# Performance work log

Hardware: AMD Instinct MI355X
Metric: run time of the kernel (lower is better)

## Reference

```python
import jax, jax.numpy as jnp
import numpy as np

EPS = 1e-5


def spectral_conv3d(x, w):
    # x: [B, C, X, Y, Z] real; w: [4, Cin, Cout, m1, m2, m3, 2] (4 frequency corners, real/imag)
    m1, m2, m3 = w.shape[3], w.shape[4], w.shape[5]
    wc = w[..., 0] + 1j * w[..., 1]
    X, Y, Z = x.shape[-3], x.shape[-2], x.shape[-1]
    xf = jnp.fft.rfftn(x, axes=(-3, -2, -1), norm="ortho")  # [B,C,X,Y,Z//2+1] complex
    mul = lambda a, b: jnp.einsum('bixyz,ioxyz->boxyz', a, b)
    out = jnp.zeros(xf.shape, dtype=xf.dtype)
    out = out.at[:, :, :m1, :m2, :m3].set(mul(xf[:, :, :m1, :m2, :m3], wc[0]))
    out = out.at[:, :, -m1:, :m2, :m3].set(mul(xf[:, :, -m1:, :m2, :m3], wc[1]))
    out = out.at[:, :, :m1, -m2:, :m3].set(mul(xf[:, :, :m1, -m2:, :m3], wc[2]))
    out = out.at[:, :, -m1:, -m2:, :m3].set(mul(xf[:, :, -m1:, -m2:, :m3], wc[3]))
    return jnp.fft.irfftn(out, s=(X, Y, Z), axes=(-3, -2, -1), norm="ortho")


def batchnorm3d(x, g, b):
    # training-mode BatchNorm3d: stats over (B, X, Y, Z) per channel, biased variance
    mean = jnp.mean(x, axis=(0, 2, 3, 4), keepdims=True)
    var = jnp.var(x, axis=(0, 2, 3, 4), keepdims=True)
    xhat = (x - mean) * jax.lax.rsqrt(var + EPS)
    return xhat * g[None, :, None, None, None] + b[None, :, None, None, None]


def setup_inputs() -> dict:
    key = jax.random.key(0)
    ks = jax.random.split(key, 12)
    B, X, Y, Z = 4, 64, 64, 64
    W, M = 32, 8
    scale = 1.0 / (W * W)
    return {
        "x": jax.random.normal(ks[0], (B, X, Y, Z, 3), dtype=jnp.float32),
        "fc0_w": jax.random.normal(ks[1], (W, 3), dtype=jnp.float32) * 0.3,
        "fc0_b": jax.random.normal(ks[2], (W,), dtype=jnp.float32) * 0.1,
        "sw": scale * jax.random.uniform(ks[3], (4, 4, W, W, M, M, M, 2), dtype=jnp.float32),
        "cw": jax.random.normal(ks[4], (4, W, W), dtype=jnp.float32) * (1.0 / np.sqrt(W)),
        "cb": jax.random.normal(ks[5], (4, W), dtype=jnp.float32) * 0.05,
        "gamma": jnp.ones((4, W), dtype=jnp.float32),
        "beta": jnp.zeros((4, W), dtype=jnp.float32),
        "fc1_w": jax.random.normal(ks[6], (128, W), dtype=jnp.float32) * (1.0 / np.sqrt(W)),
        "fc1_b": jax.random.normal(ks[7], (128,), dtype=jnp.float32) * 0.05,
        "fc2_w": jax.random.normal(ks[8], (1, 128), dtype=jnp.float32) * (1.0 / np.sqrt(128.0)),
        "fc2_b": jax.random.normal(ks[9], (1,), dtype=jnp.float32) * 0.05,
    }


def reference(x, fc0_w, fc0_b, sw, cw, cb, gamma, beta, fc1_w, fc1_b, fc2_w, fc2_b):
    # lift: [B,X,Y,Z,3] -> [B,X,Y,Z,W] -> [B,W,X,Y,Z]
    h = jnp.einsum('bxyzi,wi->bxyzw', x, fc0_w) + fc0_b
    h = jnp.transpose(h, (0, 4, 1, 2, 3))
    for i in range(4):
        x1 = spectral_conv3d(h, sw[i])
        x2 = jnp.einsum('bcxyz,oc->boxyz', h, cw[i]) + cb[i][None, :, None, None, None]
        h = batchnorm3d(x1 + x2, gamma[i], beta[i])
        if i < 3:
            h = jax.nn.relu(h)
    h = jnp.transpose(h, (0, 2, 3, 4, 1))  # [B,X,Y,Z,W]
    h = jax.nn.relu(jnp.einsum('bxyzw,fw->bxyzf', h, fc1_w) + fc1_b)
    out = jnp.einsum('bxyzf,of->bxyzo', h, fc2_w) + fc2_b
    return out
```

## Files before the change

### kernel.cpp

```cpp
#include <hip/hip_runtime.h>

#define TW_STEP 0.09817477042468103f

typedef __bf16 bf16x8 __attribute__((ext_vector_type(8)));
typedef __bf16 bf16x4 __attribute__((ext_vector_type(4)));
typedef __bf16 bf16x2 __attribute__((ext_vector_type(2)));
typedef float  f32x4  __attribute__((ext_vector_type(4)));

static constexpr size_t SZ_P   = (size_t)4*32*64*64*64*2;
static constexpr size_t SZ_A   = (size_t)4*32*8*64*64*8;
static constexpr size_t SZ_B2  = (size_t)4*32*8*16*64*8;
static constexpr size_t SZ_XF  = (size_t)4*32*8*16*16*8;
static constexpr size_t OFF_P  = 0;
static constexpr size_t OFF_A  = OFF_P + SZ_P;
static constexpr size_t OFF_B2 = OFF_A + SZ_A;
static constexpr size_t OFF_XF = OFF_B2 + SZ_B2;
static constexpr size_t OFF_YF = OFF_XF + SZ_XF;
static constexpr size_t OFF_TW  = OFF_YF + SZ_XF;
static constexpr size_t OFF_BNP = OFF_TW + 512;
static constexpr size_t OFF_W1B = OFF_BNP + 1024;
static constexpr size_t OFF_B1P = OFF_W1B + 8192;
static constexpr size_t OFF_WFZ = OFF_B1P + 512;
static constexpr size_t OFF_WZ  = OFF_WFZ + 4096;
static constexpr size_t OFF_WY  = OFF_WZ + 8192;


__global__ void k_twinit(float2* tw, __bf16* wfz, __bf16* wz, __bf16* wy) {
    int t = threadIdx.x;
    if (t < 64) { float s, c; sincosf(TW_STEP * t, &s, &c); tw[t] = make_float2(c, s); }
    for (int e = t; e < 1024; e += 256) {
        int half = e >> 9, rem = e & 511, kg = rem >> 7, tt = (rem >> 3) & 15, j = e & 7;
        int z = half * 32 + kg * 8 + j, k = tt >> 1;
        float ang = TW_STEP * (float)((k * z) & 63);
        float val = (tt & 1) ? -sinf(ang) : cosf(ang);
        __bf16 hi = (__bf16)val;
        wfz[e] = hi;
        wfz[1024 + e] = (__bf16)(val - (float)hi);
    }
    for (int e = t; e < 2048; e += 256) {
        int z = e >> 5, tt = e & 31, k = tt >> 1;
        float ang = TW_STEP * (float)((k * z) & 63);
        float val;
        if (tt == 0) val = 1.f;
        else if (tt == 1) val = 0.f;
        else val = (tt & 1) ? (-2.f * sinf(ang)) : (2.f * cosf(ang));
        __bf16 hi = (__bf16)val;
        wz[e] = hi;
        wz[2048 + e] = (__bf16)(val - (float)hi);
    }
    for (int e = t; e < 4096; e += 256) {
        int j = e & 7, l = (e >> 3) & 63, hl = (e >> 9) & 1, nt = (e >> 10) & 1, kc = (e >> 11) & 1;
        int f = l & 15;
        int F = f < 8 ? f : f + 48;
        int y = kc * 32 + ((l >> 4) & 3) * 8 + j;
        float ang = TW_STEP * (float)((F * y) & 63);
        float val = nt ? sinf(ang) : cosf(ang);
        __bf16 hi = (__bf16)val;
        wy[e] = hl ? (__bf16)(val - (float)hi) : hi;
    }
}

__global__ __launch_bounds__(256) void k_lift(const float* __restrict__ x,
                                              const float* __restrict__ w,
                                              const float* __restrict__ bias,
                                              __bf16* __restrict__ P) {
    int v = blockIdx.x * 256 + threadIdx.x;
    int z = v & 63, y = (v >> 6) & 63, xx = (v >> 12) & 63, b = v >> 18;
    float i0 = x[(size_t)v * 3 + 0], i1 = x[(size_t)v * 3 + 1], i2 = x[(size_t)v * 3 + 2];
#pragma unroll
    for (int c = 0; c < 32; c++) {
        float val = bias[c] + w[c * 3 + 0] * i0 + w[c * 3 + 1] * i1 + w[c * 3 + 2] * i2;
        P[(size_t)(((b * 32 + c) * 64 + xx) * 64 + y) * 64 + z] = (__bf16)val;
    }
}

__global__ __launch_bounds__(256) void k_zfwd2(const __bf16* __restrict__ P,
                                               const __bf16* __restrict__ wfz,
                                               const __bf16* __restrict__ wy,
                                               const float* __restrict__ bnp, int relu,
                                               unsigned* __restrict__ T2u) {
    int blk = blockIdx.x;
    int x = blk & 63, c = (blk >> 6) & 31, b = blk >> 11;
    __shared__ __bf16 hs2buf[64][72];
    __shared__ float ttmp[16][66];
    __shared__ __bf16 af[16][72];
    float (*ddsh)[2][16][18] = (float(*)[2][16][18])hs2buf;
    int tid = threadIdx.x, l = tid & 63, w = tid >> 6;
    {
        int y = tid >> 2, q = tid & 3;
        float scb = 1.f, shb = 0.f;
        if (bnp) { scb = bnp[c]; shb = bnp[32 + c]; }
        const __bf16* src = P + ((size_t)((b * 32 + c) * 64 + x) * 64 + y) * 64 + q * 16;
        bf16x8 v0 = ((const bf16x8*)src)[0], v1 = ((const bf16x8*)src)[1];
        bf16x8 o0, o1;
#pragma unroll
        for (int j = 0; j < 8; j++) {
            float a = (float)v0[j], bb = (float)v1[j];
            if (bnp) {
                a = fmaf(a, scb, shb); bb = fmaf(bb, scb, shb);
                if (relu) { a = fmaxf(a, 0.f); bb = fmaxf(bb, 0.f); }
            }
            o0[j] = (__bf16)a; o1[j] = (__bf16)bb;
        }
        *(bf16x8*)&hs2buf[y][q * 16] = o0;
        *(bf16x8*)&hs2buf[y][q * 16 + 8] = o1;
    }
    __syncthreads();
    int col = l & 15, kg = l >> 4;
    {
        f32x4 acc = (f32x4){0.f, 0.f, 0.f, 0.f};
#pragma unroll
        for (int half = 0; half < 2; half++) {
            bf16x8 a = *(const bf16x8*)&hs2buf[w * 16 + col][half * 32 + kg * 8];
            const __bf16* wp = wfz + ((half * 4 + kg) * 16 + col) * 8;
            bf16x8 bh = *(const bf16x8*)wp;
            bf16x8 blo = *(const bf16x8*)(wp + 1024);
            acc = __builtin_amdgcn_mfma_f32_16x16x32_bf16(a, bh, acc, 0, 0, 0);
            acc = __builtin_amdgcn_mfma_f32_16x16x32_bf16(a, blo, acc, 0, 0, 0);
        }
#pragma unroll
        for (int r = 0; r < 4; r++) ttmp[col][w * 16 + kg * 4 + r] = acc[r];
    }
    __syncthreads();
    {
        int row = tid >> 4, yq = tid & 15;
        float v0 = ttmp[row][yq * 4 + 0];
        float v1 = ttmp[row][yq * 4 + 1];
        float v2 = ttmp[row][yq * 4 + 2];
        float v3 = ttmp[row][yq * 4 + 3];
        bf16x4 o;
        o[0] = (__bf16)v0; o[1] = (__bf16)v1; o[2] = (__bf16)v2; o[3] = (__bf16)v3;
        *(bf16x4*)&af[row][yq * 4] = o;
    }
    __syncthreads();
    {
        int nt = w & 1, kc = w >> 1;
        bf16x8 a = *(const bf16x8*)&af[col][kc * 32 + kg * 8];
        const __bf16* wp = wy + (kc * 2 + nt) * 1024 + l * 8;
        bf16x8 bh = *(const bf16x8*)wp;
        bf16x8 blo = *(const bf16x8*)(wp + 512);
        f32x4 d = (f32x4){0.f, 0.f, 0.f, 0.f};
        d = __builtin_amdgcn_mfma_f32_16x16x32_bf16(a, bh, d, 0, 0, 0);
        d = __builtin_amdgcn_mfma_f32_16x16x32_bf16(a, blo, d, 0, 0, 0);
#pragma unroll
        for (int r = 0; r < 4; r++) ddsh[kc][nt][kg * 4 + r][col] = d[r];
    }
    __syncthreads();
    if (tid < 128) {
        int kz = tid >> 4, f = tid & 15;
        int tre = 2 * kz, tim = 2 * kz + 1;
        float Re = (ddsh[0][0][tre][f] + ddsh[1][0][tre][f])
                 + (ddsh[0][1][tim][f] + ddsh[1][1][tim][f]);
        float Im = (ddsh[0][0][tim][f] + ddsh[1][0][tim][f])
                 - (ddsh[0][1][tre][f] + ddsh[1][1][tre][f]);
        union { __bf16 h[2]; unsigned u; } pk;
        pk.h[0] = (__bf16)Re; pk.h[1] = (__bf16)Im;
        T2u[(size_t)((b * 32 + c) * 8 + kz) * 1024 + f * 64 + x] = pk.u;
    }
}

__global__ __launch_bounds__(256) void k_dftm(const __bf16* __restrict__ in,
                                              float2* __restrict__ outf,
                                              const __bf16* __restrict__ wy) {
    int rb = blockIdx.x * 16;
    __shared__ __bf16 af[32 * 72];
    __shared__ float dd[2][2][16][18];
    int tid = threadIdx.x, l = tid & 63, w = tid >> 6;
    {
        int r = tid >> 4, yq = tid & 15;
        bf16x8 v = *(const bf16x8*)(in + ((size_t)(rb + r) * 64 + yq * 4) * 2);
        bf16x4 re, im;
#pragma unroll
        for (int j = 0; j < 4; j++) { re[j] = v[2 * j]; im[j] = v[2 * j + 1]; }
        *(bf16x4*)&af[(2 * r) * 72 + yq * 4] = re;
        *(bf16x4*)&af[(2 * r + 1) * 72 + yq * 4] = im;
    }
    __syncthreads();
    int mt = w >> 1, nt = w & 1, col = l & 15, kg = l >> 4;
    f32x4 acc = (f32x4){0.f, 0.f, 0.f, 0.f};
#pragma unroll
    for (int kc = 0; kc < 2; kc++) {
        bf16x8 a = *(const bf16x8*)&af[(mt * 16 + col) * 72 + kc * 32 + kg * 8];
        const __bf16* wp = wy + (kc * 2 + nt) * 1024 + l * 8;
        bf16x8 bh = *(const bf16x8*)wp;
        bf16x8 blo = *(const bf16x8*)(wp + 512);
        acc = __builtin_amdgcn_mfma_f32_16x16x32_bf16(a, bh, acc, 0, 0, 0);
        acc = __builtin_amdgcn_mfma_f32_16x16x32_bf16(a, blo, acc, 0, 0, 0);
    }
#pragma unroll
    for (int r = 0; r < 4; r++) dd[mt][nt][kg * 4 + r][col] = acc[r];
    __syncthreads();
    {
        int cr = tid >> 4, f = tid & 15;
        int mt2 = cr >> 3, tre = (2 * cr) & 15, tim = (2 * cr + 1) & 15;
        float Re = dd[mt2][0][tre][f] + dd[mt2][1][tim][f];
        float Im = dd[mt2][0][tim][f] - dd[mt2][1][tre][f];
        int rg = rb + cr;
        outf[rg * 16 + f] = make_float2(Re, Im);
    }
}

__global__ __launch_bounds__(128) void k_specmul(const float2* __restrict__ Xf,
                                                 const float* __restrict__ swl,
                                                 float2* __restrict__ Yf) {
    int m = blockIdx.x;
    int kxi = m & 15, kyi = (m >> 4) & 15, kz = m >> 8;
    int corner = (kxi >= 8 ? 1 : 0) + (kyi >= 8 ? 2 : 0);
    int mx = kxi & 7, my = kyi & 7;
    __shared__ float2 wsd[1024];
    __shared__ float2 xfs[128];
    int tid = threadIdx.x;
    const float* wb = swl + (size_t)corner * 1048576 + mx * 128 + my * 16 + kz * 2;
    for (int idx = tid; idx < 1024; idx += 128) {
        int i = idx >> 5, o = idx & 31;
        const float* p = wb + (size_t)i * 32768 + o * 1024;
        wsd[idx] = make_float2(p[0], p[1]);
    }
    {
        int b = tid >> 5, i = tid & 31;
        xfs[tid] = Xf[(((b * 32 + i) * 8 + kz) * 16 + kyi) * 16 + kxi];
    }
    __syncthreads();
    int b = tid >> 5, o = tid & 31;
    float ar = 0.f, ai = 0.f;
#pragma unroll
    for (int i = 0; i < 32; i++) {
        float2 xv = xfs[b * 32 + i];
        float2 wv = wsd[i * 32 + o];
        ar += xv.x * wv.x - xv.y * wv.y;
        ai += xv.x * wv.y + xv.y * wv.x;
    }
    const float s = 1.0f / 262144.0f;
    Yf[(((b * 32 + o) * 8 + kz) * 16 + kyi) * 16 + kxi] = make_float2(ar * s, ai * s);
}

__global__ __launch_bounds__(256) void k_xinv(const float2* __restrict__ Yf,
                                              unsigned* __restrict__ U1p) {
    int blk = blockIdx.x;
    int kz = blk & 7, o = (blk >> 3) & 31, b = blk >> 8;
    __shared__ float2 yfs[16][17];
    __shared__ float2 tw[64];
    int tid = threadIdx.x;
    if (tid < 64) { float s, c; sincosf(TW_STEP * tid, &s, &c); tw[tid] = make_float2(c, s); }
    {
        int kyi = tid >> 4, kxi = tid & 15;
        yfs[kyi][kxi] = Yf[(size_t)((b * 32 + o) * 8 + kz) * 256 + tid];
    }
    __syncthreads();
    size_t base = (size_t)((b * 8 + kz) * 64) * 512 + o;
#pragma unroll
    for (int r = 0; r < 4; r++) {
        int idx = tid + r * 256;
        int x = idx >> 4, kyi = idx & 15;
        float ar = 0.f, ai = 0.f;
#pragma unroll
        for (int kxi = 0; kxi < 16; kxi++) {
            int f = kxi < 8 ? kxi : kxi + 48;
            float2 t = tw[(f * x) & 63];
            float2 v = yfs[kyi][kxi];
            ar += v.x * t.x - v.y * t.y;
            ai += v.x * t.y + v.y * t.x;
        }
        union { __bf16 h[2]; unsigned u; } pk;
        pk.h[0] = (__bf16)ar; pk.h[1] = (__bf16)ai;
        U1p[base + (size_t)x * 512 + kyi * 32] = pk.u;
    }
}

__global__ __launch_bounds__(256) void k_fuse(__bf16* __restrict__ P,
                                              const unsigned* __restrict__ U1p,
                                              const float* __restrict__ cwl,
                                              const float* __restrict__ cbl,
                                              const __bf16* __restrict__ wz,
                                              const float* __restrict__ bnp, int relu,
                                              float* __restrict__ part) {
    int blk = blockIdx.x;
    int yt = blk >> 8, bxi = blk & 255;
    int b = bxi >> 6, x = bxi & 63;
    int y0 = yt * 4;
    __shared__ __bf16 hs[256 * 40];
    __shared__ __bf16 u2b[4][32][20];
    __shared__ float2 twl[64];
    __shared__ float sredS[4][32], sredQ[4][32];
    int tid = threadIdx.x;
    int l = tid & 63, w = tid >> 6;
    if (tid < 64) { float s, c; sincosf(TW_STEP * tid, &s, &c); twl[tid] = make_float2(c, s); }
    __syncthreads();

    int col = l & 15, kg = l >> 4;
    bf16x8 cwf[2];
    float cbv[2];
#pragma unroll
    for (int nt = 0; nt < 2; nt++) {
        int o = nt * 16 + col;
        const float4* p4 = (const float4*)(cwl + o * 32 + kg * 8);
        float4 q0 = p4[0], q1 = p4[1];
        cwf[nt][0] = (__bf16)q0.x; cwf[nt][1] = (__bf16)q0.y;
        cwf[nt][2] = (__bf16)q0.z; cwf[nt][3] = (__bf16)q0.w;
        cwf[nt][4] = (__bf16)q1.x; cwf[nt][5] = (__bf16)q1.y;
        cwf[nt][6] = (__bf16)q1.z; cwf[nt][7] = (__bf16)q1.w;
        cbv[nt] = cbl[o];
    }

    {
        int c = tid >> 3, j = tid & 7;
        float scb = 1.f, shb = 0.f;
        if (bnp) { scb = bnp[c]; shb = bnp[32 + c]; }
        const __bf16* src = P + ((size_t)((b * 32 + c) * 64 + x) * 64 + y0) * 64 + j * 8;
#pragma unroll
        for (int q = 0; q < 4; q++) {
            bf16x8 v8 = *(const bf16x8*)(src + q * 64);
            float fv[8];
#pragma unroll
            for (int jj = 0; jj < 8; jj++) {
                float v = (float)v8[jj];
                if (bnp) { v = fmaf(v, scb, shb); if (relu) v = fmaxf(v, 0.f); }
                fv[jj] = v;
            }
#pragma unroll
            for (int s = 0; s < 8; s++) {
                int jr = (s + j) & 7;
                hs[(q * 64 + j * 8 + jr) * 40 + c] = (__bf16)fv[jr];
            }
        }
    }
    {
        int o = tid & 31, kz = tid >> 5;
        const unsigned* u1p = U1p + (size_t)((b * 8 + kz) * 64 + x) * 512 + o;
        float ur[16], ui[16];
#pragma unroll
        for (int kyi = 0; kyi < 16; kyi++) {
            union { unsigned u; __bf16 h[2]; } pk;
            pk.u = u1p[kyi * 32];
            ur[kyi] = (float)pk.h[0]; ui[kyi] = (float)pk.h[1];
        }
        float spr[8], sdr[8], spi[8], sdi[8];
#pragma unroll
        for (int p = 1; p < 8; p++) {
            spr[p] = ur[p] + ur[16 - p]; sdr[p] = ur[p] - ur[16 - p];
            spi[p] = ui[p] + ui[16 - p]; sdi[p] = ui[p] - ui[16 - p];
        }
#pragma unroll
        for (int yy = 0; yy < 4; yy++) {
            int y = y0 + yy;
            float arv = ur[0], aiv = ui[0];
            float2 t8 = twl[(8 * y) & 63];
            arv = fmaf(ur[8], t8.x, arv); arv = fmaf(ui[8], t8.y, arv);
            aiv = fmaf(ui[8], t8.x, aiv); aiv = fmaf(-ur[8], t8.y, aiv);
#pragma unroll
            for (int p = 1; p < 8; p++) {
                float2 t = twl[(p * y) & 63];
                arv = fmaf(spr[p], t.x, arv); arv = fmaf(-sdi[p], t.y, arv);
                aiv = fmaf(spi[p], t.x, aiv); aiv = fmaf(sdr[p], t.y, aiv);
            }
            union { __bf16 h[2]; unsigned u; } pk;
            pk.h[0] = (__bf16)arv; pk.h[1] = (__bf16)aiv;
            *(unsigned*)&u2b[yy][o][2 * kz] = pk.u;
        }
    }
    __syncthreads();

    f32x4 acc[4][2];
#pragma unroll
    for (int i = 0; i < 4; i++) {
        bf16x8 a = *(const bf16x8*)&hs[((w * 4 + i) * 16 + col) * 40 + kg * 8];
#pragma unroll
        for (int nt = 0; nt < 2; nt++) {
            acc[i][nt] = (f32x4){0.f, 0.f, 0.f, 0.f};
            acc[i][nt] = __builtin_amdgcn_mfma_f32_16x16x32_bf16(a, cwf[nt], acc[i][nt], 0, 0, 0);
        }
    }
    {
        bf16x8 u2f[2];
#pragma unroll
        for (int nt = 0; nt < 2; nt++) {
            bf16x8 v = (bf16x8){(__bf16)0.f, (__bf16)0.f, (__bf16)0.f, (__bf16)0.f,
                                (__bf16)0.f, (__bf16)0.f, (__bf16)0.f, (__bf16)0.f};
            if (kg < 2) {
                bf16x4 lo = *(const bf16x4*)&u2b[w][nt * 16 + col][kg * 8];
                bf16x4 hi = *(const bf16x4*)&u2b[w][nt * 16 + col][kg * 8 + 4];
                v[0] = lo[0]; v[1] = lo[1]; v[2] = lo[2]; v[3] = lo[3];
                v[4] = hi[0]; v[5] = hi[1]; v[6] = hi[2]; v[7] = hi[3];
            }
            u2f[nt] = v;
        }
#pragma unroll
        for (int i = 0; i < 4; i++) {
            int z = i * 16 + col;
            const __bf16* wp = wz + z * 32 + kg * 8;
            bf16x8 wzh = *(const bf16x8*)wp;
            bf16x8 wzl = *(const bf16x8*)(wp + 2048);
#pragma unroll
            for (int nt = 0; nt < 2; nt++) {
                acc[i][nt] = __builtin_amdgcn_mfma_f32_16x16x32_bf16(wzh, u2f[nt], acc[i][nt], 0, 0, 0);
                acc[i][nt] = __builtin_amdgcn_mfma_f32_16x16x32_bf16(wzl, u2f[nt], acc[i][nt], 0, 0, 0);
            }
        }
    }

    float sacc[2] = {0.f, 0.f}, ssacc[2] = {0.f, 0.f};
#pragma unroll
    for (int nt = 0; nt < 2; nt++) {
        int o = nt * 16 + col;
        __bf16* dstb = P + ((size_t)((b * 32 + o) * 64 + x) * 64 + (y0 + w)) * 64;
#pragma unroll
        for (int i = 0; i < 4; i++) {
            int z0s = i * 16 + kg * 4;
            bf16x4 outv;
#pragma unroll
            for (int r = 0; r < 4; r++) {
                float f = acc[i][nt][r] + cbv[nt];
                sacc[nt] += f;
                ssacc[nt] = fmaf(f, f, ssacc[nt]);
                outv[r] = (__bf16)f;
            }
            *(bf16x4*)(dstb + z0s) = outv;
        }
    }
#pragma unroll
    for (int nt = 0; nt < 2; nt++) {
        sacc[nt] += __shfl_xor(sacc[nt], 16, 64);
        sacc[nt] += __shfl_xor(sacc[nt], 32, 64);
        ssacc[nt] += __shfl_xor(ssacc[nt], 16, 64);
        ssacc[nt] += __shfl_xor(ssacc[nt], 32, 64);
    }
    if (l < 16) {
        sredS[w][col] = sacc[0]; sredS[w][16 + col] = sacc[1];
        sredQ[w][col] = ssacc[0]; sredQ[w][16 + col] = ssacc[1];
    }
    __syncthreads();
    if (tid < 32) {
        float S = sredS[0][tid] + sredS[1][tid] + sredS[2][tid] + sredS[3][tid];
        float SS = sredQ[0][tid] + sredQ[1][tid] + sredQ[2][tid] + sredQ[3][tid];
        part[((size_t)tid * 4096 + blk) * 2 + 0] = S;
        part[((size_t)tid * 4096 + blk) * 2 + 1] = SS;
    }
}

__global__ __launch_bounds__(256) void k_red2(const float* __restrict__ part,
                                              const float* __restrict__ gamma,
                                              const float* __restrict__ beta,
                                              float* __restrict__ bnp) {
    int c = blockIdx.x;
    int tid = threadIdx.x;
    const float2* pc = (const float2*)(part + (size_t)c * 8192);
    float s = 0.f, ss = 0.f;
#pragma unroll
    for (int q = 0; q < 16; q++) { float2 v = pc[tid * 16 + q]; s += v.x; ss += v.y; }
#pragma unroll
    for (int d = 32; d; d >>= 1) { s += __shfl_down(s, d, 64); ss += __shfl_down(ss, d, 64); }
    __shared__ float ws[8];
    if ((tid & 63) == 0) { ws[(tid >> 6) * 2] = s; ws[(tid >> 6) * 2 + 1] = ss; }
    __syncthreads();
    if (tid == 0) {
        double S = (double)ws[0] + ws[2] + ws[4] + ws[6];
        double SS = (double)ws[1] + ws[3] + ws[5] + ws[7];
        const double invN = 1.0 / 1048576.0;
        double mean = S * invN;
        double var = SS * invN - mean * mean;
        float scl = gamma[c] * rsqrtf((float)var + 1e-5f);
        bnp[c] = scl;
        bnp[32 + c] = beta[c] - (float)mean * scl;
    }
}

__global__ void k_prep(const float* __restrict__ w1, const float* __restrict__ b1,
                       const float* __restrict__ bnp,
                       __bf16* __restrict__ w1b, float* __restrict__ b1p) {
    int f = threadIdx.x;
    if (f >= 128) return;
    float acc = b1[f];
#pragma unroll
    for (int c = 0; c < 32; c++) {
        float wv = w1[f * 32 + c];
        w1b[f * 32 + c] = (__bf16)(wv * bnp[c]);
        acc = fmaf(wv, bnp[32 + c], acc);
    }
    b1p[f] = acc;
}

__global__ __launch_bounds__(256) void k_head(const __bf16* __restrict__ P,
                                              const __bf16* __restrict__ w1b,
                                              const float* __restrict__ b1p,
                                              const float* __restrict__ w2,
                                              const float* __restrict__ b2,
                                              float* __restrict__ out) {
    __shared__ __bf16 hs[64 * 40];
    int tid = threadIdx.x;
    int b = blockIdx.x >> 9;
    int r0 = (blockIdx.x & 511) * 512;
    int l = tid & 63;
    int w = tid >> 6;
    int col = l & 15, kg = l >> 4, hi = l >> 4;

    bf16x8 afr[8];
    f32x4 b1q[8], w2q[8];
    {
#pragma unroll
        for (int nt = 0; nt < 8; nt++) {
            afr[nt] = *(const bf16x8*)(w1b + (nt * 16 + col) * 32 + kg * 8);
            b1q[nt] = ((const f32x4*)b1p)[nt * 4 + hi];
            w2q[nt] = ((const f32x4*)w2)[nt * 4 + hi];
        }
    }
    float b2v = b2[0];
    int sc_c = tid & 31, sc_j = tid >> 5;
    const __bf16* srcb = P + (size_t)(b * 32 + sc_c) * 262144 + r0 + sc_j * 8;

    for (int t = 0; t < 8; t++) {
        {
            bf16x8 v8 = *(const bf16x8*)(srcb + t * 64);
#pragma unroll
            for (int s = 0; s < 8; s++) {
                int jr = (s + sc_j * 4) & 7;
                hs[(sc_j * 8 + jr) * 40 + sc_c] = v8[jr];
            }
        }
        __syncthreads();
        bf16x8 hfr = *(const bf16x8*)&hs[(w * 16 + col) * 40 + kg * 8];
        f32x4 acc[8];
#pragma unroll
        for (int nt = 0; nt < 8; nt++) {
            acc[nt] = (f32x4){0.f, 0.f, 0.f, 0.f};
            acc[nt] = __builtin_amdgcn_mfma_f32_16x16x32_bf16(afr[nt], hfr, acc[nt], 0, 0, 0);
        }
        float s = 0.f;
#pragma unroll
        for (int nt = 0; nt < 8; nt++) {
#pragma unroll
            for (int r = 0; r < 4; r++) {
                float val = fmaxf(acc[nt][r] + b1q[nt][r], 0.f);
                s = fmaf(w2q[nt][r], val, s);
            }
        }
        s += __shfl_xor(s, 16, 64);
        s += __shfl_xor(s, 32, 64);
        if (l < 16)
            out[b * 262144 + r0 + t * 64 + w * 16 + l] = s + b2v;
        __syncthreads();
    }
}

extern "C" void kernel_launch(void* const* d_in, const int* in_sizes, int n_in,
                              void* d_out, int out_size, void* d_ws, size_t ws_size,
                              hipStream_t stream) {
    const float* x     = (const float*)d_in[0];
    const float* fc0_w = (const float*)d_in[1];
    const float* fc0_b = (const float*)d_in[2];
    const float* sw    = (const float*)d_in[3];
    const float* cw    = (const float*)d_in[4];
    const float* cb    = (const float*)d_in[5];
    const float* gamma = (const float*)d_in[6];
    const float* beta  = (const float*)d_in[7];
    const float* fc1_w = (const float*)d_in[8];
    const float* fc1_b = (const float*)d_in[9];
    const float* fc2_w = (const float*)d_in[10];
    const float* fc2_b = (const float*)d_in[11];

    char* ws = (char*)d_ws;
    __bf16* P    = (__bf16*)(ws + OFF_P);
    __bf16* T2b  = (__bf16*)(ws + OFF_B2);
    unsigned* T2u = (unsigned*)(ws + OFF_B2);
    unsigned* U1p = (unsigned*)(ws + OFF_B2);
    float2* Xf   = (float2*)(ws + OFF_XF);
    float2* Yf   = (float2*)(ws + OFF_YF);
    float*  part = (float*)(ws + OFF_XF);
    float2* gtw  = (float2*)(ws + OFF_TW);
    float*  bnp  = (float*)(ws + OFF_BNP);
    __bf16* w1b  = (__bf16*)(ws + OFF_W1B);
    float*  b1p  = (float*)(ws + OFF_B1P);
    __bf16* wfz  = (__bf16*)(ws + OFF_WFZ);
    __bf16* wz   = (__bf16*)(ws + OFF_WZ);
    __bf16* wy   = (__bf16*)(ws + OFF_WY);

    k_twinit<<<1, 256, 0, stream>>>(gtw, wfz, wz, wy);
    k_lift<<<4096, 256, 0, stream>>>(x, fc0_w, fc0_b, P);

    for (int i = 0; i < 4; i++) {
        const float* bprev = (i == 0) ? nullptr : (bnp + (i - 1) * 64);
        int relu = (i > 0) ? 1 : 0;
        k_zfwd2<<<8192, 256, 0, stream>>>(P, wfz, wy, bprev, relu, T2u);
        k_dftm<<<1024, 256, 0, stream>>>(T2b, Xf, wy);
        k_specmul<<<2048, 128, 0, stream>>>(Xf, sw + (size_t)i * 4194304, Yf);
        k_xinv<<<1024, 256, 0, stream>>>(Yf, U1p);
        k_fuse<<<4096, 256, 0, stream>>>(P, U1p, cw + i * 1024, cb + i * 32, wz, bprev, relu, part);
        k_red2<<<32, 256, 0, stream>>>(part, gamma + i * 32, beta + i * 32, bnp + i * 64);
    }

    k_prep<<<1, 128, 0, stream>>>(fc1_w, fc1_b, bnp + 3 * 64, w1b, b1p);
    k_head<<<2048, 256, 0, stream>>>(P, w1b, b1p, fc2_w, fc2_b, (float*)d_out);
}
```

Measured before the change: 417.9 us.

## Split k_fuse work across 512 threads, one output-channel half per wave

Doubles the k_fuse block size to 512 threads. Each of the 8 waves now handles one y row and one 16-channel half instead of both halves. The staging loads, the y-direction inverse DFT and the BN partial sums are split across the extra threads to match. The goal is more parallelism and fewer live registers per thread to hide latency. In exchange, each block repeats the hs A-fragment loads and the wz weight loads once per channel half.

```diff
diff --git a/kernel.cpp b/kernel.cpp
--- a/kernel.cpp
+++ b/kernel.cpp
@@ -267,7 +267,7 @@
     }
 }
 
-__global__ __launch_bounds__(256) void k_fuse(__bf16* __restrict__ P,
+__global__ __launch_bounds__(512) void k_fuse(__bf16* __restrict__ P,
                                               const unsigned* __restrict__ U1p,
                                               const float* __restrict__ cwl,
                                               const float* __restrict__ cbl,
@@ -281,34 +281,35 @@
     __shared__ __bf16 hs[256 * 40];
     __shared__ __bf16 u2b[4][32][20];
     __shared__ float2 twl[64];
-    __shared__ float sredS[4][32], sredQ[4][32];
+    __shared__ float sredS[8][16], sredQ[8][16];
     int tid = threadIdx.x;
     int l = tid & 63, w = tid >> 6;
     if (tid < 64) { float s, c; sincosf(TW_STEP * tid, &s, &c); twl[tid] = make_float2(c, s); }
     __syncthreads();
 
     int col = l & 15, kg = l >> 4;
-    bf16x8 cwf[2];
-    float cbv[2];
-#pragma unroll
-    for (int nt = 0; nt < 2; nt++) {
-        int o = nt * 16 + col;
+    int w2 = w >> 2, wy = w & 3;
+    bf16x8 cwf;
+    float cbv;
+    {
+        int o = w2 * 16 + col;
         const float4* p4 = (const float4*)(cwl + o * 32 + kg * 8);
         float4 q0 = p4[0], q1 = p4[1];
-        cwf[nt][0] = (__bf16)q0.x; cwf[nt][1] = (__bf16)q0.y;
-        cwf[nt][2] = (__bf16)q0.z; cwf[nt][3] = (__bf16)q0.w;
-        cwf[nt][4] = (__bf16)q1.x; cwf[nt][5] = (__bf16)q1.y;
-        cwf[nt][6] = (__bf16)q1.z; cwf[nt][7] = (__bf16)q1.w;
-        cbv[nt] = cbl[o];
-    }
-
-    {
-        int c = tid >> 3, j = tid & 7;
+        cwf[0] = (__bf16)q0.x; cwf[1] = (__bf16)q0.y;
+        cwf[2] = (__bf16)q0.z; cwf[3] = (__bf16)q0.w;
+        cwf[4] = (__bf16)q1.x; cwf[5] = (__bf16)q1.y;
+        cwf[6] = (__bf16)q1.z; cwf[7] = (__bf16)q1.w;
+        cbv = cbl[o];
+    }
+
+    {
+        int c = tid >> 4, yh = (tid >> 3) & 1, j = tid & 7;
         float scb = 1.f, shb = 0.f;
         if (bnp) { scb = bnp[c]; shb = bnp[32 + c]; }
         const __bf16* src = P + ((size_t)((b * 32 + c) * 64 + x) * 64 + y0) * 64 + j * 8;
 #pragma unroll
-        for (int q = 0; q < 4; q++) {
+        for (int qq = 0; qq < 2; qq++) {
+            int q = yh * 2 + qq;
             bf16x8 v8 = *(const bf16x8*)(src + q * 64);
             float fv[8];
 #pragma unroll
@@ -325,7 +326,7 @@
         }
     }
     {
-        int o = tid & 31, kz = tid >> 5;
+        int o = tid & 31, kz = (tid >> 5) & 7, half = tid >> 8;
         const unsigned* u1p = U1p + (size_t)((b * 8 + kz) * 64 + x) * 512 + o;
         float ur[16], ui[16];
 #pragma unroll
@@ -341,7 +342,8 @@
             spi[p] = ui[p] + ui[16 - p]; sdi[p] = ui[p] - ui[16 - p];
         }
 #pragma unroll
-        for (int yy = 0; yy < 4; yy++) {
+        for (int yq = 0; yq < 2; yq++) {
+            int yy = half * 2 + yq;
             int y = y0 + yy;
             float arv = ur[0], aiv = ui[0];
             float2 t8 = twl[(8 * y) & 63];
@@ -360,29 +362,21 @@
     }
     __syncthreads();
 
-    f32x4 acc[4][2];
+    f32x4 acc[4];
 #pragma unroll
     for (int i = 0; i < 4; i++) {
-        bf16x8 a = *(const bf16x8*)&hs[((w * 4 + i) * 16 + col) * 40 + kg * 8];
-#pragma unroll
-        for (int nt = 0; nt < 2; nt++) {
-            acc[i][nt] = (f32x4){0.f, 0.f, 0.f, 0.f};
-            acc[i][nt] = __builtin_amdgcn_mfma_f32_16x16x32_bf16(a, cwf[nt], acc[i][nt], 0, 0, 0);
-        }
-    }
-    {
-        bf16x8 u2f[2];
-#pragma unroll
-        for (int nt = 0; nt < 2; nt++) {
-            bf16x8 v = (bf16x8){(__bf16)0.f, (__bf16)0.f, (__bf16)0.f, (__bf16)0.f,
-                                (__bf16)0.f, (__bf16)0.f, (__bf16)0.f, (__bf16)0.f};
-            if (kg < 2) {
-                bf16x4 lo = *(const bf16x4*)&u2b[w][nt * 16 + col][kg * 8];
-                bf16x4 hi = *(const bf16x4*)&u2b[w][nt * 16 + col][kg * 8 + 4];
-                v[0] = lo[0]; v[1] = lo[1]; v[2] = lo[2]; v[3] = lo[3];
-                v[4] = hi[0]; v[5] = hi[1]; v[6] = hi[2]; v[7] = hi[3];
-            }
-            u2f[nt] = v;
+        bf16x8 a = *(const bf16x8*)&hs[((wy * 4 + i) * 16 + col) * 40 + kg * 8];
+        acc[i] = (f32x4){0.f, 0.f, 0.f, 0.f};
+        acc[i] = __builtin_amdgcn_mfma_f32_16x16x32_bf16(a, cwf, acc[i], 0, 0, 0);
+    }
+    {
+        bf16x8 u2f = (bf16x8){(__bf16)0.f, (__bf16)0.f, (__bf16)0.f, (__bf16)0.f,
+                              (__bf16)0.f, (__bf16)0.f, (__bf16)0.f, (__bf16)0.f};
+        if (kg < 2) {
+            bf16x4 lo = *(const bf16x4*)&u2b[wy][w2 * 16 + col][kg * 8];
+            bf16x4 hi = *(const bf16x4*)&u2b[wy][w2 * 16 + col][kg * 8 + 4];
+            u2f[0] = lo[0]; u2f[1] = lo[1]; u2f[2] = lo[2]; u2f[3] = lo[3];
+            u2f[4] = hi[0]; u2f[5] = hi[1]; u2f[6] = hi[2]; u2f[7] = hi[3];
         }
 #pragma unroll
         for (int i = 0; i < 4; i++) {
@@ -390,48 +384,43 @@
             const __bf16* wp = wz + z * 32 + kg * 8;
             bf16x8 wzh = *(const bf16x8*)wp;
             bf16x8 wzl = *(const bf16x8*)(wp + 2048);
-#pragma unroll
-            for (int nt = 0; nt < 2; nt++) {
-                acc[i][nt] = __builtin_amdgcn_mfma_f32_16x16x32_bf16(wzh, u2f[nt], acc[i][nt], 0, 0, 0);
-                acc[i][nt] = __builtin_amdgcn_mfma_f32_16x16x32_bf16(wzl, u2f[nt], acc[i][nt], 0, 0, 0);
-            }
-        }
-    }
-
-    float sacc[2] = {0.f, 0.f}, ssacc[2] = {0.f, 0.f};
-#pragma unroll
-    for (int nt = 0; nt < 2; nt++) {
-        int o = nt * 16 + col;
-        __bf16* dstb = P + ((size_t)((b * 32 + o) * 64 + x) * 64 + (y0 + w)) * 64;
+            acc[i] = __builtin_amdgcn_mfma_f32_16x16x32_bf16(wzh, u2f, acc[i], 0, 0, 0);
+            acc[i] = __builtin_amdgcn_mfma_f32_16x16x32_bf16(wzl, u2f, acc[i], 0, 0, 0);
+        }
+    }
+
+    float sacc = 0.f, ssacc = 0.f;
+    {
+        int o = w2 * 16 + col;
+        __bf16* dstb = P + ((size_t)((b * 32 + o) * 64 + x) * 64 + (y0 + wy)) * 64;
 #pragma unroll
         for (int i = 0; i < 4; i++) {
             int z0s = i * 16 + kg * 4;
             bf16x4 outv;
 #pragma unroll
             for (int r = 0; r < 4; r++) {
-                float f = acc[i][nt][r] + cbv[nt];
-                sacc[nt] += f;
-                ssacc[nt] = fmaf(f, f, ssacc[nt]);
+                float f = acc[i][r] + cbv;
+                sacc += f;
+                ssacc = fmaf(f, f, ssacc);
                 outv[r] = (__bf16)f;
             }
             *(bf16x4*)(dstb + z0s) = outv;
         }
     }
-#pragma unroll
-    for (int nt = 0; nt < 2; nt++) {
-        sacc[nt] += __shfl_xor(sacc[nt], 16, 64);
-        sacc[nt] += __shfl_xor(sacc[nt], 32, 64);
-        ssacc[nt] += __shfl_xor(ssacc[nt], 16, 64);
-        ssacc[nt] += __shfl_xor(ssacc[nt], 32, 64);
-    }
-    if (l < 16) {
-        sredS[w][col] = sacc[0]; sredS[w][16 + col] = sacc[1];
-        sredQ[w][col] = ssacc[0]; sredQ[w][16 + col] = ssacc[1];
-    }
+    sacc += __shfl_xor(sacc, 16, 64);
+    sacc += __shfl_xor(sacc, 32, 64);
+    ssacc += __shfl_xor(ssacc, 16, 64);
+    ssacc += __shfl_xor(ssacc, 32, 64);
+    if (l < 16) { sredS[w][col] = sacc; sredQ[w][col] = ssacc; }
     __syncthreads();
     if (tid < 32) {
-        float S = sredS[0][tid] + sredS[1][tid] + sredS[2][tid] + sredS[3][tid];
-        float SS = sredQ[0][tid] + sredQ[1][tid] + sredQ[2][tid] + sredQ[3][tid];
+        int ch2 = tid >> 4, chc = tid & 15;
+        float S = 0.f, SS = 0.f;
+#pragma unroll
+        for (int q = 0; q < 4; q++) {
+            S += sredS[ch2 * 4 + q][chc];
+            SS += sredQ[ch2 * 4 + q][chc];
+        }
         part[((size_t)tid * 4096 + blk) * 2 + 0] = S;
         part[((size_t)tid * 4096 + blk) * 2 + 1] = SS;
     }
@@ -583,7 +572,7 @@
         k_dftm<<<1024, 256, 0, stream>>>(T2b, Xf, wy);
         k_specmul<<<2048, 128, 0, stream>>>(Xf, sw + (size_t)i * 4194304, Yf);
         k_xinv<<<1024, 256, 0, stream>>>(Yf, U1p);
-        k_fuse<<<4096, 256, 0, stream>>>(P, U1p, cw + i * 1024, cb + i * 32, wz, bprev, relu, part);
+        k_fuse<<<4096, 512, 0, stream>>>(P, U1p, cw + i * 1024, cb + i * 32, wz, bprev, relu, part);
         k_red2<<<32, 256, 0, stream>>>(part, gamma + i * 32, beta + i * 32, bnp + i * 64);
     }
 
```

Result: slower. 447.0 us (+7.0%).
